# Optimization experiments

Hardware: AMD Instinct MI355X
Metric: run time of the kernel (lower is better)

## Reference

```python
import jax, jax.numpy as jnp
import numpy as np
from jax import lax

# Config (matches init_kwargs / ModelCfg.__post_init__)
B, L = 2, 1024
D, E, N, D_DELTA, D_CONV, V, N_LAYERS = 768, 1536, 16, 48, 4, 50280, 2


def setup_inputs() -> dict:
    key = jax.random.key(0)
    ks = jax.random.split(key, 16)
    s = 0.02
    inp = {
        "tokens": jax.random.randint(ks[0], (B, L), 0, V),
        "embedding": jax.random.normal(ks[1], (V, D), jnp.float32) * s,
        "norm_w": jnp.ones((N_LAYERS, D), jnp.float32),
        "skip_w": jax.random.normal(ks[2], (N_LAYERS, E, D), jnp.float32) * s,
        "in_w": jax.random.normal(ks[3], (N_LAYERS, E, D), jnp.float32) * s,
        "conv_w": jax.random.normal(ks[4], (N_LAYERS, E, 1, D_CONV), jnp.float32) * 0.1,
        "conv_b": jax.random.normal(ks[5], (N_LAYERS, E), jnp.float32) * s,
        "Wd1": jax.random.normal(ks[6], (N_LAYERS, D_DELTA, E), jnp.float32) * s,
        "Wd2_w": jax.random.normal(ks[7], (N_LAYERS, E, D_DELTA), jnp.float32) * s,
        "Wd2_b": jax.random.normal(ks[8], (N_LAYERS, E), jnp.float32) * s,
        "WB": jax.random.normal(ks[9], (N_LAYERS, N, E), jnp.float32) * s,
        "WC": jax.random.normal(ks[10], (N_LAYERS, N, E), jnp.float32) * s,
        "A_log": jax.random.normal(ks[11], (N_LAYERS, E, N), jnp.float32) * 0.5,
        "W_D": jnp.ones((N_LAYERS, E), jnp.float32),
        "out_w": jax.random.normal(ks[12], (N_LAYERS, D, E), jnp.float32) * s,
        "final_norm_w": jnp.ones((D,), jnp.float32),
        "lm_head_w": jax.random.normal(ks[13], (V, D), jnp.float32) * s,
    }
    return inp


def rmsnorm(x, w, eps=1e-5):
    return x * lax.rsqrt(jnp.mean(x * x, axis=-1, keepdims=True) + eps) * w


def mamba_block(resid, nw, skw, inw, cw, cb, wd1, wd2w, wd2b, wb, wc, a_log, wd, ow):
    x = rmsnorm(resid, nw)                      # [B,L,D]
    skip = x @ skw.T                            # [B,L,E]
    xi = x @ inw.T                              # [B,L,E]
    # depthwise causal conv1d (left pad D_CONV-1 == torch pad + slice [:L])
    xc = lax.conv_general_dilated(
        xi.transpose(0, 2, 1), cw, window_strides=(1,),
        padding=[(D_CONV - 1, 0)], feature_group_count=E,
        dimension_numbers=("NCH", "OIH", "NCH"))
    x = jax.nn.silu((xc + cb[None, :, None]).transpose(0, 2, 1))  # [B,L,E]

    A = -jnp.exp(a_log)                                            # [E,N]
    delta = jax.nn.softplus((x @ wd1.T) @ wd2w.T + wd2b)           # [B,L,E]
    Bm = x @ wb.T                                                  # [B,L,N]
    Cm = x @ wc.T                                                  # [B,L,N]
    dA = jnp.exp(delta[..., None] * A)                             # [B,L,E,N]
    dBx = delta[..., None] * Bm[:, :, None, :] * x[..., None]      # [B,L,E,N]

    def step(h, t):
        dA_t, dBx_t, C_t = t
        h = dA_t * h + dBx_t                                       # [B,E,N]
        y = jnp.einsum("ben,bn->be", h, C_t)
        return h, y

    h0 = jnp.zeros((B, E, N), x.dtype)
    _, ys = lax.scan(step, h0, (dA.transpose(1, 0, 2, 3),
                                dBx.transpose(1, 0, 2, 3),
                                Cm.transpose(1, 0, 2)))
    y = ys.transpose(1, 0, 2)                                      # [B,L,E]
    y = (y + x * wd) * jax.nn.silu(skip)
    return resid + y @ ow.T


def reference(tokens, embedding, norm_w, skip_w, in_w, conv_w, conv_b, Wd1,
              Wd2_w, Wd2_b, WB, WC, A_log, W_D, out_w, final_norm_w, lm_head_w):
    resid = embedding[tokens]                                      # [B,L,D]
    for i in range(N_LAYERS):
        resid = mamba_block(resid, norm_w[i], skip_w[i], in_w[i], conv_w[i],
                            conv_b[i], Wd1[i], Wd2_w[i], Wd2_b[i], WB[i],
                            WC[i], A_log[i], W_D[i], out_w[i])
    resid = rmsnorm(resid, final_norm_w)
    logits = resid @ lm_head_w.T                                   # [B,L,V]
    return logits
```

## Files before the change

### kernel.cpp

```cpp
#include <hip/hip_runtime.h>
#include <hip/hip_bf16.h>

#define BB     2
#define LL     1024
#define BL     (BB*LL)
#define BDIM   768
#define EDIM   1536
#define NST    16
#define DDELTA 48
#define DDPAD  64
#define DCONV  4
#define VOCAB  50280
#define NLAYERS 2

#define CCH    16
#define TCH    (LL/CCH)
#define BEN    (BB*EDIM*NST)

typedef __hip_bfloat16 bf16;
typedef short short8 __attribute__((ext_vector_type(8)));
typedef float floatx4 __attribute__((ext_vector_type(4)));

static __device__ __forceinline__ float bf2f(bf16 v){ return __bfloat162float(v); }
static __device__ __forceinline__ bf16  f2bf(float v){ return __float2bfloat16(v); }

typedef const __attribute__((address_space(1))) unsigned int gu32;
typedef __attribute__((address_space(3))) unsigned int lu32;
static __device__ __forceinline__ void glds16(const bf16* g, bf16* l) {
  __builtin_amdgcn_global_load_lds((gu32*)g, (lu32*)l, 16, 0, 0);
}

__global__ void k_cvt(const float* __restrict__ src, bf16* __restrict__ dst) {
  int idx = blockIdx.x*256 + threadIdx.x;
  dst[idx] = f2bf(src[idx]);
}

__global__ void k_embed(const int* __restrict__ tok, const float* __restrict__ emb,
                        float* __restrict__ resid) {
  int idx = blockIdx.x*256 + threadIdx.x;
  int bl = idx / BDIM, d = idx % BDIM;
  resid[idx] = emb[(size_t)tok[bl]*BDIM + d];
}

__global__ __launch_bounds__(256) void k_rmsnorm(const float* __restrict__ resid,
                        const float* __restrict__ w, bf16* __restrict__ out) {
  int m = blockIdx.x, tid = threadIdx.x;
  const float* row = resid + (size_t)m*BDIM;
  float ss = 0.f;
  for (int d = tid; d < BDIM; d += 256) { float v = row[d]; ss += v*v; }
  for (int off = 32; off; off >>= 1) ss += __shfl_down(ss, off);
  __shared__ float red[4];
  if ((tid & 63) == 0) red[tid>>6] = ss;
  __syncthreads();
  float rstd = rsqrtf((red[0]+red[1]+red[2]+red[3]) / (float)BDIM + 1e-5f);
  for (int d = tid; d < BDIM; d += 256)
    out[(size_t)m*BDIM + d] = f2bf(row[d]*rstd*w[d]);
}

template<bool OUT_BF16>
__global__ __launch_bounds__(256) void k_gemm(const bf16* __restrict__ A,
      const bf16* __restrict__ W, void* __restrict__ Cp, int N, int K) {
  __shared__ alignas(16) bf16 As[128*32];
  __shared__ alignas(16) bf16 Bs[128*32];
  const int nwg = gridDim.x * gridDim.y;
  const int orig = blockIdx.y * gridDim.x + blockIdx.x;
  const int qq = nwg >> 3, rr = nwg & 7;
  const int xcd = orig & 7, sub = orig >> 3;
  const int logical = (xcd < rr ? xcd*(qq+1) : rr*(qq+1) + (xcd-rr)*qq) + sub;
  const int by = logical % gridDim.y;
  const int bx = logical / gridDim.y;
  const int m0 = by * 128, n0 = bx * 128;

  const int tid = threadIdx.x, lane = tid & 63, wave = tid >> 6;
  const int wm = (wave >> 1) * 64, wn = (wave & 1) * 64;
  const int mr = lane & 15, q = lane >> 4;
  floatx4 acc[4][4] = {};

  const int sr = lane >> 2, ch = lane & 3;
  const int wbase = wave * 16;
  int wr0 = n0 + wbase + sr;      if (wr0 >= N) wr0 = N - 1;
  int wr1 = n0 + 64 + wbase + sr; if (wr1 >= N) wr1 = N - 1;
  const bf16* Ar0 = A + (size_t)(m0 + wbase + sr)*K      + ch*8;
  const bf16* Ar1 = A + (size_t)(m0 + 64 + wbase + sr)*K + ch*8;
  const bf16* Wr0 = W + (size_t)wr0*K + ch*8;
  const bf16* Wr1 = W + (size_t)wr1*K + ch*8;
  bf16* lA0 = As + wbase*32;
  bf16* lA1 = As + (64 + wbase)*32;
  bf16* lB0 = Bs + wbase*32;
  bf16* lB1 = Bs + (64 + wbase)*32;

  for (int k0 = 0; k0 < K; k0 += 32) {
    __syncthreads();
    glds16(Ar0 + k0, lA0);
    glds16(Ar1 + k0, lA1);
    glds16(Wr0 + k0, lB0);
    glds16(Wr1 + k0, lB1);
    asm volatile("s_waitcnt vmcnt(0)" ::: "memory");
    __syncthreads();
    short8 af[4], bfr[4];
    #pragma unroll
    for (int i = 0; i < 4; i++)
      af[i]  = *reinterpret_cast<const short8*>(&As[(wm + i*16 + mr)*32 + q*8]);
    #pragma unroll
    for (int j = 0; j < 4; j++)
      bfr[j] = *reinterpret_cast<const short8*>(&Bs[(wn + j*16 + mr)*32 + q*8]);
    #pragma unroll
    for (int i = 0; i < 4; i++)
      #pragma unroll
      for (int j = 0; j < 4; j++)
        acc[i][j] = __builtin_amdgcn_mfma_f32_16x16x32_bf16(af[i], bfr[j], acc[i][j], 0, 0, 0);
  }
  #pragma unroll
  for (int i = 0; i < 4; i++)
    #pragma unroll
    for (int j = 0; j < 4; j++)
      #pragma unroll
      for (int rg = 0; rg < 4; rg++) {
        int m = m0 + wm + i*16 + q*4 + rg;
        int n = n0 + wn + j*16 + mr;
        if (n < N) {
          float v = acc[i][j][rg];
          if (OUT_BF16) ((bf16*)Cp)[(size_t)m*N + n] = f2bf(v);
          else          ((float*)Cp)[(size_t)m*N + n] = v;
        }
      }
}

__global__ void k_conv(const float* __restrict__ xi, const float* __restrict__ cw,
                       const float* __restrict__ cb, float* __restrict__ xc) {
  int idx = blockIdx.x*256 + threadIdx.x;
  int e = idx % EDIM, bl = idx / EDIM, l = bl % LL;
  float acc = cb[e];
  #pragma unroll
  for (int k = 0; k < DCONV; k++) {
    int ls = l - (DCONV-1) + k;
    if (ls >= 0) acc += xi[(size_t)(bl + ls - l)*EDIM + e] * cw[e*DCONV + k];
  }
  xc[idx] = acc / (1.f + expf(-acc));
}

__global__ __launch_bounds__(256) void k_d1(const float* __restrict__ xc,
      const float* __restrict__ wd1, bf16* __restrict__ d1) {
  int m = blockIdx.x, tid = threadIdx.x;
  __shared__ float xrow[EDIM];
  for (int k = tid; k < EDIM; k += 256) xrow[k] = xc[(size_t)m*EDIM + k];
  __syncthreads();
  int wave = tid >> 6, lane = tid & 63;
  for (int n = wave; n < DDPAD; n += 4) {
    float s = 0.f;
    if (n < DDELTA) {
      const float* wr = wd1 + (size_t)n*EDIM;
      for (int k = lane; k < EDIM; k += 64) s += xrow[k]*wr[k];
      for (int off = 32; off; off >>= 1) s += __shfl_down(s, off);
    }
    if (lane == 0) d1[(size_t)m*DDPAD + n] = f2bf(s);
  }
}

__global__ void k_padw(const float* __restrict__ wsrc, bf16* __restrict__ wp) {
  int idx = blockIdx.x*256 + threadIdx.x;
  int e = idx >> 6, cc = idx & 63;
  wp[idx] = (cc < DDELTA) ? f2bf(wsrc[(size_t)e*DDELTA + cc]) : f2bf(0.f);
}

__global__ void k_softplus(float* __restrict__ d, const float* __restrict__ b) {
  int idx = blockIdx.x*256 + threadIdx.x;
  int e = idx % EDIM;
  float v = d[idx] + b[e];
  d[idx] = fmaxf(v, 0.f) + log1pf(expf(-fabsf(v)));
}

__global__ __launch_bounds__(256) void k_bc(const float* __restrict__ xc,
    const float* __restrict__ wb, const float* __restrict__ wc,
    float* __restrict__ Bm, float* __restrict__ Cm) {
  int m = blockIdx.x, tid = threadIdx.x;
  __shared__ float xrow[EDIM];
  for (int k = tid; k < EDIM; k += 256) xrow[k] = xc[(size_t)m*EDIM + k];
  __syncthreads();
  int wave = tid >> 6, lane = tid & 63;
  for (int n = wave; n < 32; n += 4) {
    const float* wr = (n < NST) ? wb + (size_t)n*EDIM : wc + (size_t)(n-NST)*EDIM;
    float s = 0.f;
    for (int k = lane; k < EDIM; k += 64) s += xrow[k]*wr[k];
    for (int off = 32; off; off >>= 1) s += __shfl_down(s, off);
    if (lane == 0) {
      if (n < NST) Bm[(size_t)m*NST + n]       = s;
      else         Cm[(size_t)m*NST + (n-NST)] = s;
    }
  }
}


__global__ __launch_bounds__(256) void k_scan1(const float* __restrict__ delta,
    const float* __restrict__ xc, const float* __restrict__ Bm,
    const float* __restrict__ a_log, float* __restrict__ Pbuf,
    float* __restrict__ Hbuf) {
  int tid = threadIdx.x;
  int n = tid & 15, el = tid >> 4;
  int bx = blockIdx.x;
  int et = bx % (EDIM/16); bx /= (EDIM/16);
  int c = bx % CCH, b = bx / CCH;
  int e = et*16 + el;
  float Aen = -__expf(a_log[(size_t)e*NST + n]);
  const float* dp = delta + ((size_t)b*LL + (size_t)c*TCH)*EDIM + e;
  const float* xp = xc    + ((size_t)b*LL + (size_t)c*TCH)*EDIM + e;
  const float* bp = Bm    + ((size_t)b*LL + (size_t)c*TCH)*NST + n;
  float h = 0.f, p = 1.f;
  #pragma unroll 4
  for (int t = 0; t < TCH; t++) {
    float dl = dp[(size_t)t*EDIM];
    float xv = xp[(size_t)t*EDIM];
    float bv = bp[t*NST];
    float a = __expf(dl*Aen);
    h = a*h + dl*bv*xv;
    p *= a;
  }
  size_t ben = ((size_t)b*EDIM + e)*NST + n;
  Pbuf[(size_t)c*BEN + ben] = p;
  Hbuf[(size_t)c*BEN + ben] = h;
}

__global__ __launch_bounds__(256) void k_scanfix(const float* __restrict__ Pbuf,
    const float* __restrict__ Hbuf, float* __restrict__ Hin) {
  int ben = blockIdx.x*256 + threadIdx.x;
  float h = 0.f;
  #pragma unroll
  for (int c = 0; c < CCH; c++) {
    Hin[(size_t)c*BEN + ben] = h;
    h = Pbuf[(size_t)c*BEN + ben]*h + Hbuf[(size_t)c*BEN + ben];
  }
}

__global__ __launch_bounds__(256) void k_scan2(const float* __restrict__ delta,
    const float* __restrict__ xc, const float* __restrict__ Bm,
    const float* __restrict__ Cm, const float* __restrict__ a_log,
    const float* __restrict__ Hin, float* __restrict__ y) {
  int tid = threadIdx.x;
  int n = tid & 15, el = tid >> 4;
  int bx = blockIdx.x;
  int et = bx % (EDIM/16); bx /= (EDIM/16);
  int c = bx % CCH, b = bx / CCH;
  int e = et*16 + el;
  float Aen = -__expf(a_log[(size_t)e*NST + n]);
  const float* dp = delta + ((size_t)b*LL + (size_t)c*TCH)*EDIM + e;
  const float* xp = xc    + ((size_t)b*LL + (size_t)c*TCH)*EDIM + e;
  const float* bp = Bm    + ((size_t)b*LL + (size_t)c*TCH)*NST + n;
  const float* cp = Cm    + ((size_t)b*LL + (size_t)c*TCH)*NST + n;
  float* yp = y + ((size_t)b*LL + (size_t)c*TCH)*EDIM + e;
  size_t ben = ((size_t)b*EDIM + e)*NST + n;
  float h = Hin[(size_t)c*BEN + ben];
  #pragma unroll 4
  for (int t = 0; t < TCH; t++) {
    float dl = dp[(size_t)t*EDIM];
    float xv = xp[(size_t)t*EDIM];
    float bv = bp[t*NST];
    float cv = cp[t*NST];
    h = __expf(dl*Aen)*h + dl*bv*xv;
    float p = h*cv;
    p += __shfl_xor(p, 1); p += __shfl_xor(p, 2);
    p += __shfl_xor(p, 4); p += __shfl_xor(p, 8);
    if (n == 0) yp[(size_t)t*EDIM] = p;
  }
}

__global__ void k_ymix(const float* __restrict__ y, const float* __restrict__ xc,
    const float* __restrict__ skip, const float* __restrict__ wd, bf16* __restrict__ y2) {
  int idx = blockIdx.x*256 + threadIdx.x;
  int e = idx % EDIM;
  float s = skip[idx];
  y2[idx] = f2bf((y[idx] + xc[idx]*wd[e]) * (s / (1.f + expf(-s))));
}

__global__ void k_add(float* __restrict__ resid, const float* __restrict__ d) {
  int idx = blockIdx.x*256 + threadIdx.x;
  resid[idx] += d[idx];
}

extern "C" void kernel_launch(void* const* d_in, const int* in_sizes, int n_in,
                              void* d_out, int out_size, void* d_ws, size_t ws_size,
                              hipStream_t stream) {
  const int*   tokens = (const int*)  d_in[0];
  const float* emb    = (const float*)d_in[1];
  const float* norm_w = (const float*)d_in[2];
  const float* skip_w = (const float*)d_in[3];
  const float* in_w   = (const float*)d_in[4];
  const float* conv_w = (const float*)d_in[5];
  const float* conv_b = (const float*)d_in[6];
  const float* Wd1    = (const float*)d_in[7];
  const float* Wd2w   = (const float*)d_in[8];
  const float* Wd2b   = (const float*)d_in[9];
  const float* WBw    = (const float*)d_in[10];
  const float* WCw    = (const float*)d_in[11];
  const float* A_log  = (const float*)d_in[12];
  const float* W_D    = (const float*)d_in[13];
  const float* out_w  = (const float*)d_in[14];
  const float* fnw    = (const float*)d_in[15];
  const float* lm_w   = (const float*)d_in[16];
  float* out = (float*)d_out;

  char* wsp = (char*)d_ws;
  auto alloc = [&](size_t bytes) { char* p = wsp; wsp += (bytes + 255) & ~(size_t)255; return p; };
  float* resid = (float*)alloc((size_t)BL*BDIM*4);
  bf16*  xn    = (bf16*) alloc((size_t)BL*BDIM*2);
  float* skip  = (float*)alloc((size_t)BL*EDIM*4);
  float* xi    = (float*)alloc((size_t)BL*EDIM*4);
  float* xc    = (float*)alloc((size_t)BL*EDIM*4);
  float* dlt   = (float*)alloc((size_t)BL*EDIM*4);
  bf16*  d1    = (bf16*) alloc((size_t)BL*DDPAD*2);
  bf16*  w2p   = (bf16*) alloc((size_t)EDIM*DDPAD*2);
  float* Bm    = (float*)alloc((size_t)BL*NST*4);
  float* Cm    = (float*)alloc((size_t)BL*NST*4);
  bf16*  y2    = (bf16*) alloc((size_t)BL*EDIM*2);
  float* Pbuf  = (float*)alloc((size_t)CCH*BEN*4);
  float* Hbuf  = (float*)alloc((size_t)CCH*BEN*4);
  float* Hin   = (float*)alloc((size_t)CCH*BEN*4);
  bf16*  wcvt  = (bf16*) alloc((size_t)VOCAB*BDIM*2);

  dim3 blk(256);
  const int nED = EDIM*BDIM/256;
  const int scanGrid = BB*CCH*(EDIM/16);
  k_embed<<<BL*BDIM/256, blk, 0, stream>>>(tokens, emb, resid);
  for (int l = 0; l < NLAYERS; l++) {
    k_rmsnorm<<<BL, blk, 0, stream>>>(resid, norm_w + (size_t)l*BDIM, xn);

    k_cvt<<<nED, blk, 0, stream>>>(skip_w + (size_t)l*EDIM*BDIM, wcvt);
    k_gemm<false><<<dim3(EDIM/128, BL/128), blk, 0, stream>>>(xn, wcvt, skip, EDIM, BDIM);

    k_cvt<<<nED, blk, 0, stream>>>(in_w + (size_t)l*EDIM*BDIM, wcvt);
    k_gemm<false><<<dim3(EDIM/128, BL/128), blk, 0, stream>>>(xn, wcvt, xi, EDIM, BDIM);

    k_conv<<<BL*EDIM/256, blk, 0, stream>>>(
        xi, conv_w + (size_t)l*EDIM*DCONV, conv_b + (size_t)l*EDIM, xc);
    k_d1<<<BL, blk, 0, stream>>>(xc, Wd1 + (size_t)l*DDELTA*EDIM, d1);
    k_padw<<<EDIM*DDPAD/256, blk, 0, stream>>>(Wd2w + (size_t)l*EDIM*DDELTA, w2p);
    k_gemm<false><<<dim3(EDIM/128, BL/128), blk, 0, stream>>>(d1, w2p, dlt, EDIM, DDPAD);
    k_softplus<<<BL*EDIM/256, blk, 0, stream>>>(dlt, Wd2b + (size_t)l*EDIM);
    k_bc<<<BL, blk, 0, stream>>>(xc, WBw + (size_t)l*NST*EDIM, WCw + (size_t)l*NST*EDIM, Bm, Cm);

    k_scan1<<<scanGrid, blk, 0, stream>>>(dlt, xc, Bm,
        A_log + (size_t)l*EDIM*NST, Pbuf, Hbuf);
    k_scanfix<<<BEN/256, blk, 0, stream>>>(Pbuf, Hbuf, Hin);
    k_scan2<<<scanGrid, blk, 0, stream>>>(dlt, xc, Bm, Cm,
        A_log + (size_t)l*EDIM*NST, Hin, xi);

    k_ymix<<<BL*EDIM/256, blk, 0, stream>>>(xi, xc, skip, W_D + (size_t)l*EDIM, y2);

    k_cvt<<<nED, blk, 0, stream>>>(out_w + (size_t)l*BDIM*EDIM, wcvt);
    k_gemm<false><<<dim3(BDIM/128, BL/128), blk, 0, stream>>>(
        y2, wcvt, dlt, BDIM, EDIM);
    k_add<<<BL*BDIM/256, blk, 0, stream>>>(resid, dlt);
  }
  k_rmsnorm<<<BL, blk, 0, stream>>>(resid, fnw, xn);
  k_cvt<<<VOCAB*BDIM/256, blk, 0, stream>>>(lm_w, wcvt);
  k_gemm<false><<<dim3((VOCAB+127)/128, BL/128), blk, 0, stream>>>(
      xn, wcvt, out, VOCAB, BDIM);
}
```

Baseline: 1.664 ms.

## Fuse fp32-to-bf16 weight conversion into double-buffered swizzled GEMM

Drops the separate weight conversion kernels. The GEMM now loads fp32 weights directly, packs them to bf16 in registers and stores them into LDS. LDS is double-buffered with prefetch of the next K tile, and an XOR swizzle is added to reduce bank conflicts. This removes a full write and re-read of the large lm_head weight in bf16, at the cost of reading fp32 weights (twice the bytes) inside the GEMM and extra conversion ALU work.

```diff
diff --git a/kernel.cpp b/kernel.cpp
--- a/kernel.cpp
+++ b/kernel.cpp
@@ -21,18 +21,21 @@
 typedef short short8 __attribute__((ext_vector_type(8)));
 typedef float floatx4 __attribute__((ext_vector_type(4)));
 
-static __device__ __forceinline__ float bf2f(bf16 v){ return __bfloat162float(v); }
 static __device__ __forceinline__ bf16  f2bf(float v){ return __float2bfloat16(v); }
+static __device__ __forceinline__ short f2bs(float v){
+  bf16 b = f2bf(v); return *reinterpret_cast<short*>(&b);
+}
+static __device__ __forceinline__ short8 pack_bf16(float4 a, float4 b){
+  short8 r;
+  r[0]=f2bs(a.x); r[1]=f2bs(a.y); r[2]=f2bs(a.z); r[3]=f2bs(a.w);
+  r[4]=f2bs(b.x); r[5]=f2bs(b.y); r[6]=f2bs(b.z); r[7]=f2bs(b.w);
+  return r;
+}
 
 typedef const __attribute__((address_space(1))) unsigned int gu32;
 typedef __attribute__((address_space(3))) unsigned int lu32;
 static __device__ __forceinline__ void glds16(const bf16* g, bf16* l) {
   __builtin_amdgcn_global_load_lds((gu32*)g, (lu32*)l, 16, 0, 0);
-}
-
-__global__ void k_cvt(const float* __restrict__ src, bf16* __restrict__ dst) {
-  int idx = blockIdx.x*256 + threadIdx.x;
-  dst[idx] = f2bf(src[idx]);
 }
 
 __global__ void k_embed(const int* __restrict__ tok, const float* __restrict__ emb,
@@ -59,9 +62,9 @@
 
 template<bool OUT_BF16>
 __global__ __launch_bounds__(256) void k_gemm(const bf16* __restrict__ A,
-      const bf16* __restrict__ W, void* __restrict__ Cp, int N, int K) {
-  __shared__ alignas(16) bf16 As[128*32];
-  __shared__ alignas(16) bf16 Bs[128*32];
+      const float* __restrict__ W, void* __restrict__ Cp, int N, int K) {
+  __shared__ alignas(16) bf16 As[2][128*32];
+  __shared__ alignas(16) bf16 Bs[2][128*32];
   const int nwg = gridDim.x * gridDim.y;
   const int orig = blockIdx.y * gridDim.x + blockIdx.x;
   const int qq = nwg >> 3, rr = nwg & 7;
@@ -78,32 +81,49 @@
 
   const int sr = lane >> 2, ch = lane & 3;
   const int wbase = wave * 16;
-  int wr0 = n0 + wbase + sr;      if (wr0 >= N) wr0 = N - 1;
-  int wr1 = n0 + 64 + wbase + sr; if (wr1 >= N) wr1 = N - 1;
-  const bf16* Ar0 = A + (size_t)(m0 + wbase + sr)*K      + ch*8;
-  const bf16* Ar1 = A + (size_t)(m0 + 64 + wbase + sr)*K + ch*8;
-  const bf16* Wr0 = W + (size_t)wr0*K + ch*8;
-  const bf16* Wr1 = W + (size_t)wr1*K + ch*8;
-  bf16* lA0 = As + wbase*32;
-  bf16* lA1 = As + (64 + wbase)*32;
-  bf16* lB0 = Bs + wbase*32;
-  bf16* lB1 = Bs + (64 + wbase)*32;
-
-  for (int k0 = 0; k0 < K; k0 += 32) {
-    __syncthreads();
-    glds16(Ar0 + k0, lA0);
-    glds16(Ar1 + k0, lA1);
-    glds16(Wr0 + k0, lB0);
-    glds16(Wr1 + k0, lB1);
+  const int sA = (sr >> 1) & 3;
+  const bf16* Ar0 = A + (size_t)(m0 + wbase + sr)*K      + (ch ^ sA)*8;
+  const bf16* Ar1 = A + (size_t)(m0 + 64 + wbase + sr)*K + (ch ^ sA)*8;
+
+  const int wrow = tid >> 2, wc = tid & 3;
+  const int sW = (wrow >> 1) & 3;
+  int gn0 = n0 + wrow;      if (gn0 >= N) gn0 = N - 1;
+  int gn1 = n0 + 64 + wrow; if (gn1 >= N) gn1 = N - 1;
+  const float* Wp0 = W + (size_t)gn0*K + (wc ^ sW)*8;
+  const float* Wp1 = W + (size_t)gn1*K + (wc ^ sW)*8;
+
+  const int nt = K >> 5;
+  float4 wA0, wA1, wB0, wB1;
+
+  glds16(Ar0, &As[0][wbase*32]);
+  glds16(Ar1, &As[0][(64+wbase)*32]);
+  wA0 = *(const float4*)(Wp0);  wA1 = *(const float4*)(Wp0 + 4);
+  wB0 = *(const float4*)(Wp1);  wB1 = *(const float4*)(Wp1 + 4);
+
+  const int swq = (q ^ ((mr >> 1) & 3)) * 8;
+
+  for (int t = 0; t < nt; ++t) {
+    const int cur = t & 1;
     asm volatile("s_waitcnt vmcnt(0)" ::: "memory");
-    __syncthreads();
+    *reinterpret_cast<short8*>(&Bs[cur][wrow*32      + wc*8]) = pack_bf16(wA0, wA1);
+    *reinterpret_cast<short8*>(&Bs[cur][(64+wrow)*32 + wc*8]) = pack_bf16(wB0, wB1);
+    asm volatile("s_waitcnt lgkmcnt(0)" ::: "memory");
+    __builtin_amdgcn_s_barrier();
+    if (t + 1 < nt) {
+      const int k0 = (t + 1) * 32;
+      glds16(Ar0 + k0, &As[cur^1][wbase*32]);
+      glds16(Ar1 + k0, &As[cur^1][(64+wbase)*32]);
+      wA0 = *(const float4*)(Wp0 + k0);  wA1 = *(const float4*)(Wp0 + k0 + 4);
+      wB0 = *(const float4*)(Wp1 + k0);  wB1 = *(const float4*)(Wp1 + k0 + 4);
+    }
+    asm volatile("" ::: "memory");
     short8 af[4], bfr[4];
     #pragma unroll
     for (int i = 0; i < 4; i++)
-      af[i]  = *reinterpret_cast<const short8*>(&As[(wm + i*16 + mr)*32 + q*8]);
+      af[i]  = *reinterpret_cast<const short8*>(&As[cur][(wm + i*16 + mr)*32 + swq]);
     #pragma unroll
     for (int j = 0; j < 4; j++)
-      bfr[j] = *reinterpret_cast<const short8*>(&Bs[(wn + j*16 + mr)*32 + q*8]);
+      bfr[j] = *reinterpret_cast<const short8*>(&Bs[cur][(wn + j*16 + mr)*32 + swq]);
     #pragma unroll
     for (int i = 0; i < 4; i++)
       #pragma unroll
@@ -157,10 +177,10 @@
   }
 }
 
-__global__ void k_padw(const float* __restrict__ wsrc, bf16* __restrict__ wp) {
+__global__ void k_padw32(const float* __restrict__ wsrc, float* __restrict__ wp) {
   int idx = blockIdx.x*256 + threadIdx.x;
   int e = idx >> 6, cc = idx & 63;
-  wp[idx] = (cc < DDELTA) ? f2bf(wsrc[(size_t)e*DDELTA + cc]) : f2bf(0.f);
+  wp[idx] = (cc < DDELTA) ? wsrc[(size_t)e*DDELTA + cc] : 0.f;
 }
 
 __global__ void k_softplus(float* __restrict__ d, const float* __restrict__ b) {
@@ -307,33 +327,30 @@
   float* xc    = (float*)alloc((size_t)BL*EDIM*4);
   float* dlt   = (float*)alloc((size_t)BL*EDIM*4);
   bf16*  d1    = (bf16*) alloc((size_t)BL*DDPAD*2);
-  bf16*  w2p   = (bf16*) alloc((size_t)EDIM*DDPAD*2);
+  float* w2p32 = (float*)alloc((size_t)EDIM*DDPAD*4);
   float* Bm    = (float*)alloc((size_t)BL*NST*4);
   float* Cm    = (float*)alloc((size_t)BL*NST*4);
   bf16*  y2    = (bf16*) alloc((size_t)BL*EDIM*2);
   float* Pbuf  = (float*)alloc((size_t)CCH*BEN*4);
   float* Hbuf  = (float*)alloc((size_t)CCH*BEN*4);
   float* Hin   = (float*)alloc((size_t)CCH*BEN*4);
-  bf16*  wcvt  = (bf16*) alloc((size_t)VOCAB*BDIM*2);
 
   dim3 blk(256);
-  const int nED = EDIM*BDIM/256;
   const int scanGrid = BB*CCH*(EDIM/16);
   k_embed<<<BL*BDIM/256, blk, 0, stream>>>(tokens, emb, resid);
   for (int l = 0; l < NLAYERS; l++) {
     k_rmsnorm<<<BL, blk, 0, stream>>>(resid, norm_w + (size_t)l*BDIM, xn);
 
-    k_cvt<<<nED, blk, 0, stream>>>(skip_w + (size_t)l*EDIM*BDIM, wcvt);
-    k_gemm<false><<<dim3(EDIM/128, BL/128), blk, 0, stream>>>(xn, wcvt, skip, EDIM, BDIM);
-
-    k_cvt<<<nED, blk, 0, stream>>>(in_w + (size_t)l*EDIM*BDIM, wcvt);
-    k_gemm<false><<<dim3(EDIM/128, BL/128), blk, 0, stream>>>(xn, wcvt, xi, EDIM, BDIM);
+    k_gemm<false><<<dim3(EDIM/128, BL/128), blk, 0, stream>>>(
+        xn, skip_w + (size_t)l*EDIM*BDIM, skip, EDIM, BDIM);
+    k_gemm<false><<<dim3(EDIM/128, BL/128), blk, 0, stream>>>(
+        xn, in_w + (size_t)l*EDIM*BDIM, xi, EDIM, BDIM);
 
     k_conv<<<BL*EDIM/256, blk, 0, stream>>>(
         xi, conv_w + (size_t)l*EDIM*DCONV, conv_b + (size_t)l*EDIM, xc);
     k_d1<<<BL, blk, 0, stream>>>(xc, Wd1 + (size_t)l*DDELTA*EDIM, d1);
-    k_padw<<<EDIM*DDPAD/256, blk, 0, stream>>>(Wd2w + (size_t)l*EDIM*DDELTA, w2p);
-    k_gemm<false><<<dim3(EDIM/128, BL/128), blk, 0, stream>>>(d1, w2p, dlt, EDIM, DDPAD);
+    k_padw32<<<EDIM*DDPAD/256, blk, 0, stream>>>(Wd2w + (size_t)l*EDIM*DDELTA, w2p32);
+    k_gemm<false><<<dim3(EDIM/128, BL/128), blk, 0, stream>>>(d1, w2p32, dlt, EDIM, DDPAD);
     k_softplus<<<BL*EDIM/256, blk, 0, stream>>>(dlt, Wd2b + (size_t)l*EDIM);
     k_bc<<<BL, blk, 0, stream>>>(xc, WBw + (size_t)l*NST*EDIM, WCw + (size_t)l*NST*EDIM, Bm, Cm);
 
@@ -345,13 +362,11 @@
 
     k_ymix<<<BL*EDIM/256, blk, 0, stream>>>(xi, xc, skip, W_D + (size_t)l*EDIM, y2);
 
-    k_cvt<<<nED, blk, 0, stream>>>(out_w + (size_t)l*BDIM*EDIM, wcvt);
     k_gemm<false><<<dim3(BDIM/128, BL/128), blk, 0, stream>>>(
-        y2, wcvt, dlt, BDIM, EDIM);
+        y2, out_w + (size_t)l*BDIM*EDIM, dlt, BDIM, EDIM);
     k_add<<<BL*BDIM/256, blk, 0, stream>>>(resid, dlt);
   }
   k_rmsnorm<<<BL, blk, 0, stream>>>(resid, fnw, xn);
-  k_cvt<<<VOCAB*BDIM/256, blk, 0, stream>>>(lm_w, wcvt);
   k_gemm<false><<<dim3((VOCAB+127)/128, BL/128), blk, 0, stream>>>(
-      xn, wcvt, out, VOCAB, BDIM);
-}
+      xn, lm_w, out, VOCAB, BDIM);
+}
```

After: 1.694 ms. No clear change (+1.8%).
